# Kernel tuning notes

Measured on AMD Instinct MI355X. Metric: run time of the kernel, lower is better.

The kernel has to match this reference:

```python
import jax, jax.numpy as jnp
import numpy as np

HEAD_DIM = 128  # dim // num_heads; RoPE rot_dim and softmax scale
ROPE_THETA = 10000.0


def rope_rotate(x, rot_dim):
    # lucidrains RotaryEmbedding.rotate_queries_or_keys: rotate first rot_dim
    # channels of last axis with interleaved-pair rotation; pass rest through.
    T = x.shape[-2]
    inv_freq = 1.0 / (ROPE_THETA ** (jnp.arange(0, rot_dim, 2, dtype=jnp.float32) / rot_dim))
    freqs = jnp.arange(T, dtype=jnp.float32)[:, None] * inv_freq[None, :]  # [T, rot_dim//2]
    freqs = jnp.repeat(freqs, 2, axis=-1)  # [T, rot_dim] interleaved (f0,f0,f1,f1,...)
    cos, sin = jnp.cos(freqs), jnp.sin(freqs)
    xr, x_pass = x[..., :rot_dim], x[..., rot_dim:]
    x1, x2 = xr[..., 0::2], xr[..., 1::2]
    rot = jnp.stack([-x2, x1], axis=-1).reshape(xr.shape)  # rotate_half
    xr = xr * cos + rot * sin
    return jnp.concatenate([xr, x_pass], axis=-1)


def setup_inputs() -> dict:
    key = jax.random.key(0)
    ks = jax.random.split(key, 9)
    B, T, D = 2, 2048, 2048
    w = lambda k, shape: jax.random.normal(k, shape, dtype=jnp.float32) * 0.02
    return {
        "latent_space": jax.random.normal(ks[0], (B, T, D), dtype=jnp.float32),
        "Wq": w(ks[1], (D, D)), "bq": w(ks[2], (D,)),
        "Wk": w(ks[3], (D, D)), "bk": w(ks[4], (D,)),
        "Wv": w(ks[5], (D, D)), "bv": w(ks[6], (D,)),
        "Wfc": w(ks[7], (D, D)), "bfc": w(ks[8], (D,)),
    }


def reference(latent_space, Wq, bq, Wk, bk, Wv, bv, Wfc, bfc):
    # Projections (nn.Linear: x @ W.T + b)
    Q = latent_space @ Wq.T + bq
    K = latent_space @ Wk.T + bk
    V = latent_space @ Wv.T + bv
    # Fused RoPE on first HEAD_DIM channels (module never splits heads)
    Q = rope_rotate(Q, HEAD_DIM)
    K = rope_rotate(K, HEAD_DIM)
    # Full-hidden-dim QK^T: [B,T,T]
    qk = jnp.einsum('btd,bsd->bts', Q, K)
    T = qk.shape[-1]
    causal = jnp.triu(jnp.ones((T, T), dtype=bool), 1)
    A = jnp.where(causal, -jnp.inf, qk)
    # PartialSoftmax with temp=1, h_t=None: state = A/sqrt(head_dim);
    # out = exp(state)/sum(exp(state)) * 2
    state = A / jnp.sqrt(jnp.float32(HEAD_DIM))
    x_exp = jnp.exp(state)
    A = x_exp / jnp.sum(x_exp, axis=-1, keepdims=True) * 2.0
    out = jnp.einsum('bts,bsd->btd', A, V) @ Wfc.T + bfc
    return out
```

## Files before the change

kernel.cpp:

```cpp
#include <hip/hip_runtime.h>
#include <hip/hip_bf16.h>
#include <math.h>

using bf16 = __hip_bfloat16;
typedef __attribute__((ext_vector_type(8))) __bf16 bf16x8;
typedef __attribute__((ext_vector_type(4))) float f32x4;

static __device__ __forceinline__ void gload16(const bf16* g, bf16* l) {
  __builtin_amdgcn_global_load_lds((const __attribute__((address_space(1))) void*)g,
                                   (__attribute__((address_space(3))) void*)l, 16, 0, 0);
}

struct POff { long a[4]; long b[4]; long c[4]; const float* bias[4]; };
struct CvtP { const float* s[5]; bf16* d[5]; int n4[5]; };

__global__ __launch_bounds__(256) void cvt_f32_bf16(CvtP p) {
  const int y = blockIdx.y;
  const int i = blockIdx.x * 256 + threadIdx.x;
  if (i >= p.n4[y]) return;
  const float4 v = reinterpret_cast<const float4*>(p.s[y])[i];
  union { bf16 h[4]; short4 s4; } u;
  u.h[0] = __float2bfloat16(v.x);
  u.h[1] = __float2bfloat16(v.y);
  u.h[2] = __float2bfloat16(v.z);
  u.h[3] = __float2bfloat16(v.w);
  *reinterpret_cast<short4*>(p.d[y] + 4 * (size_t)i) = u.s4;
}

template<bool BIAS, bool F32OUT, bool CAUSAL, bool KTRUNC>
__global__ __launch_bounds__(256, 4) void gemm_nt(
    const bf16* __restrict__ A, const bf16* __restrict__ B, char* __restrict__ Cv,
    POff P, int K, int lda, int ldb, int ldc)
{
  if (CAUSAL && blockIdx.x > blockIdx.y) return;
  const int z = blockIdx.z;
  A = (const bf16*)((const char*)A + P.a[z]);
  B = (const bf16*)((const char*)B + P.b[z]);
  char* C = Cv + P.c[z];
  const int by = KTRUNC ? (gridDim.y - 1 - blockIdx.y) : blockIdx.y;
  const int rowBase = by * 128;
  const int colBase = blockIdx.x * 128;
  const int tid  = threadIdx.x;
  const int lane = tid & 63;
  const int wid  = tid >> 6;
  const int wR = (wid >> 1) * 64;
  const int wC = (wid & 1) * 64;

  __shared__ alignas(16) bf16 lsA[128 * 32];
  __shared__ alignas(16) bf16 lsB[128 * 32];

  f32x4 acc[4][4] = {};

  const int kEnd = KTRUNC ? (rowBase + 128) : K;
  const int rt = tid >> 2;
  const int cs = tid & 3;
  const int srcOff = (cs ^ ((rt >> 1) & 3)) * 8;
  const bf16* gA = A + (size_t)(rowBase + rt) * lda + srcOff;
  const bf16* gB = B + (size_t)(colBase + rt) * ldb + srcOff;
  const int lr = lane >> 4;
  const int lc = lane & 15;
  const int kb = (lr ^ ((lc >> 1) & 3)) * 8;

  for (int k0 = 0; k0 < kEnd; k0 += 32) {
    gload16(gA + k0,                    &lsA[tid * 8]);
    gload16(gA + (size_t)64 * lda + k0, &lsA[2048 + tid * 8]);
    gload16(gB + k0,                    &lsB[tid * 8]);
    gload16(gB + (size_t)64 * ldb + k0, &lsB[2048 + tid * 8]);
    __syncthreads();

    bf16x8 af[4], bf_[4];
#pragma unroll
    for (int m = 0; m < 4; ++m)
      af[m] = *reinterpret_cast<const bf16x8*>(&lsA[(wR + m * 16 + lc) * 32 + kb]);
#pragma unroll
    for (int n = 0; n < 4; ++n)
      bf_[n] = *reinterpret_cast<const bf16x8*>(&lsB[(wC + n * 16 + lc) * 32 + kb]);

#pragma unroll
    for (int m = 0; m < 4; ++m)
#pragma unroll
      for (int n = 0; n < 4; ++n)
        acc[m][n] = __builtin_amdgcn_mfma_f32_16x16x32_bf16(af[m], bf_[n], acc[m][n], 0, 0, 0);
    __syncthreads();
  }

  const float* bias = P.bias[z];
#pragma unroll
  for (int m = 0; m < 4; ++m) {
    const int row0 = rowBase + wR + m * 16 + lr * 4;
#pragma unroll
    for (int n = 0; n < 4; ++n) {
      const int col = colBase + wC + n * 16 + lc;
      const float bv = BIAS ? bias[col] : 0.f;
#pragma unroll
      for (int j = 0; j < 4; ++j) {
        const float v = acc[m][n][j] + bv;
        const long idx = (long)(row0 + j) * ldc + col;
        if (F32OUT) reinterpret_cast<float*>(C)[idx] = v;
        else        reinterpret_cast<bf16*>(C)[idx] = __float2bfloat16(v);
      }
    }
  }
}

__global__ __launch_bounds__(256) void rope_bf16(bf16* __restrict__ X) {
  const int idx = blockIdx.x * 256 + threadIdx.x;
  const int row = idx >> 6;
  const int i   = idx & 63;
  const int t   = row & 2047;
  const float ang = (float)t * exp2f((float)i * -0.20762050593046f);
  float sn, cs;
  sincosf(ang, &sn, &cs);
  bf16* p = X + ((long)row << 11) + 2 * i;
  const float x1 = __bfloat162float(p[0]);
  const float x2 = __bfloat162float(p[1]);
  p[0] = __float2bfloat16(x1 * cs - x2 * sn);
  p[1] = __float2bfloat16(x2 * cs + x1 * sn);
}

__global__ __launch_bounds__(256) void softmax_causal(
    const float* __restrict__ S0, const float* __restrict__ S1,
    const float* __restrict__ S2, const float* __restrict__ S3,
    bf16* __restrict__ A0, bf16* __restrict__ A1) {
  const int t = blockIdx.x;
  const int b = blockIdx.y;
  const float* ra = (b ? S2 : S0) + (long)t * 2048;
  const float* rb = (b ? S3 : S1) + (long)t * 2048;
  bf16* orow = (b ? A1 : A0) + (long)t * 4096;
  const int L = t + 1;
  __shared__ float e[2048];
  __shared__ float red[4];
  const float scale = 0.0883883476483184f;
  const int lane = threadIdx.x & 63, wd = threadIdx.x >> 6;

  float mx = -INFINITY;
  for (int s = threadIdx.x; s < L; s += 256) {
    const float v = (ra[s] + rb[s]) * scale;
    e[s] = v;
    mx = fmaxf(mx, v);
  }
#pragma unroll
  for (int off = 1; off < 64; off <<= 1) mx = fmaxf(mx, __shfl_xor(mx, off));
  if (lane == 0) red[wd] = mx;
  __syncthreads();
  mx = fmaxf(fmaxf(red[0], red[1]), fmaxf(red[2], red[3]));
  __syncthreads();

  float sum = 0.f;
  for (int s = threadIdx.x; s < L; s += 256) {
    const float v = expf(e[s] - mx);
    e[s] = v;
    sum += v;
  }
#pragma unroll
  for (int off = 1; off < 64; off <<= 1) sum += __shfl_xor(sum, off);
  if (lane == 0) red[wd] = sum;
  __syncthreads();
  sum = red[0] + red[1] + red[2] + red[3];
  const float f = 2.f / sum;
  for (int s = threadIdx.x; s < 2048; s += 256) {
    const float v = (s < L) ? e[s] * f : 0.f;
    orow[s] = __float2bfloat16(v);
  }
}

__global__ __launch_bounds__(256) void transpose_bf16(
    const bf16* __restrict__ V, bf16* __restrict__ VT) {
  __shared__ bf16 tile[32][33];
  const long b = blockIdx.z;
  const int s0 = blockIdx.y * 32, d0 = blockIdx.x * 32;
  const int tx = threadIdx.x;
  const int ty = threadIdx.y;
  for (int i = ty; i < 32; i += 8)
    tile[i][tx] = V[(b * 2048 + s0 + i) * 2048 + d0 + tx];
  __syncthreads();
  for (int i = ty; i < 32; i += 8)
    VT[(b * 2048 + d0 + i) * 2048 + s0 + tx] = tile[tx][i];
}

extern "C" void kernel_launch(void* const* d_in, const int* in_sizes, int n_in,
                              void* d_out, int out_size, void* d_ws, size_t ws_size,
                              hipStream_t stream) {
  (void)in_sizes; (void)n_in; (void)out_size; (void)ws_size;
  const float* lat = (const float*)d_in[0];
  const float* Wq  = (const float*)d_in[1];
  const float* bq  = (const float*)d_in[2];
  const float* Wk  = (const float*)d_in[3];
  const float* bk  = (const float*)d_in[4];
  const float* Wv  = (const float*)d_in[5];
  const float* bv  = (const float*)d_in[6];
  const float* Wfc = (const float*)d_in[7];
  const float* bfc = (const float*)d_in[8];
  float* out = (float*)d_out;

  constexpr long T = 2048, D = 2048, MT = 4096;
  constexpr long TTB = T * T * 4;
  char* w = (char*)d_ws;
  bf16* latb = (bf16*)w;  w += MT * D * 2;
  bf16* wqb  = (bf16*)w;  w += D * D * 2;
  bf16* wkb  = (bf16*)w;  w += D * D * 2;
  bf16* wvb  = (bf16*)w;  w += D * D * 2;
  bf16* wfb  = (bf16*)w;  w += D * D * 2;
  bf16* Qb   = (bf16*)w;  w += MT * D * 2;
  bf16* Kb   = (bf16*)w;  w += MT * D * 2;
  bf16* Vb   = (bf16*)w;  w += MT * D * 2;
  bf16* VTb  = (bf16*)w;  w += MT * D * 2;
  float* S0  = (float*)w; w += TTB;
  float* S1  = (float*)w; w += TTB;
  float* S2  = (float*)d_out;
  float* S3  = (float*)((char*)d_out + TTB);
  bf16* A0   = (bf16*)S0;
  bf16* A1   = (bf16*)S3;
  bf16* Ob   = latb;

  CvtP cp;
  cp.s[0] = lat; cp.d[0] = latb; cp.n4[0] = (int)(MT * D / 4);
  cp.s[1] = Wq;  cp.d[1] = wqb;  cp.n4[1] = (int)(D * D / 4);
  cp.s[2] = Wk;  cp.d[2] = wkb;  cp.n4[2] = (int)(D * D / 4);
  cp.s[3] = Wv;  cp.d[3] = wvb;  cp.n4[3] = (int)(D * D / 4);
  cp.s[4] = Wfc; cp.d[4] = wfb;  cp.n4[4] = (int)(D * D / 4);
  cvt_f32_bf16<<<dim3(8192, 5), 256, 0, stream>>>(cp);

  POff pq = {};
  for (int z = 0; z < 3; ++z) {
    pq.a[z] = 0;
    pq.b[z] = (long)z * D * D * 2;
    pq.c[z] = (long)z * MT * D * 2;
  }
  pq.bias[0] = bq; pq.bias[1] = bk; pq.bias[2] = bv;
  gemm_nt<true,false,false,false><<<dim3(16, 32, 3), 256, 0, stream>>>(
      latb, wqb, (char*)Qb, pq, 2048, 2048, 2048, 2048);

  rope_bf16<<<2048, 256, 0, stream>>>(Qb);

  POff ps = {};
  for (int z = 0; z < 4; ++z) {
    ps.a[z] = (long)(z >> 1) * T * D * 2 + (long)(z & 1) * 1024 * 2;
    ps.b[z] = ps.a[z];
  }
  ps.c[0] = 0;
  ps.c[1] = TTB;
  ps.c[2] = (char*)S2 - (char*)S0;
  ps.c[3] = (char*)S3 - (char*)S0;
  gemm_nt<false,true,true,false><<<dim3(16, 16, 4), 256, 0, stream>>>(
      Qb, Kb, (char*)S0, ps, 1024, 2048, 2048, 2048);

  softmax_causal<<<dim3(2048, 2), 256, 0, stream>>>(S0, S1, S2, S3, A0, A1);

  transpose_bf16<<<dim3(64, 64, 2), dim3(32, 8), 0, stream>>>(Vb, VTb);

  POff pv = {};
  pv.a[0] = 0; pv.a[1] = (char*)A1 - (char*)A0;
  pv.b[0] = 0; pv.b[1] = (long)D * T * 2;
  pv.c[0] = 0; pv.c[1] = (long)T * D * 2;
  gemm_nt<false,false,false,true><<<dim3(16, 16, 2), 256, 0, stream>>>(
      (const bf16*)A0, VTb, (char*)Ob, pv, 2048, 4096, 2048, 2048);

  POff pf = {};
  pf.bias[0] = bfc;
  gemm_nt<true,true,false,false><<<dim3(16, 32, 1), 256, 0, stream>>>(
      Ob, wfb, (char*)out, pf, 2048, 2048, 2048, 2048);
}
```

Measured before the change: 313.5 us.

## Pipeline GEMM with 4-stage LDS ring buffer and 256x128 tiles of 512 threads

Rewrites the shared GEMM kernel to use 512-thread blocks computing 256x128 tiles, with a 4-deep LDS ring buffer and loads issued three stages ahead. Explicit vmcnt waits and raw barriers replace the double __syncthreads per iteration, and MFMA sections run at raised wave priority. The aim is to hide global-to-LDS latency and halve B-tile loads per output. The trade-off is coarser causal skipping, more LDS per block and fewer blocks per grid.

```diff
diff --git a/kernel.cpp b/kernel.cpp
--- a/kernel.cpp
+++ b/kernel.cpp
@@ -5,6 +5,9 @@
 using bf16 = __hip_bfloat16;
 typedef __attribute__((ext_vector_type(8))) __bf16 bf16x8;
 typedef __attribute__((ext_vector_type(4))) float f32x4;
+
+#define SBAR() asm volatile("s_barrier" ::: "memory")
+#define WAITVM(n) asm volatile("s_waitcnt vmcnt(" #n ")" ::: "memory")
 
 static __device__ __forceinline__ void gload16(const bf16* g, bf16* l) {
   __builtin_amdgcn_global_load_lds((const __attribute__((address_space(1))) void*)g,
@@ -28,69 +31,81 @@
 }
 
 template<bool BIAS, bool F32OUT, bool CAUSAL, bool KTRUNC>
-__global__ __launch_bounds__(256, 4) void gemm_nt(
+__global__ __launch_bounds__(512, 2) void gemm_nt(
     const bf16* __restrict__ A, const bf16* __restrict__ B, char* __restrict__ Cv,
     POff P, int K, int lda, int ldb, int ldc)
 {
-  if (CAUSAL && blockIdx.x > blockIdx.y) return;
+  if (CAUSAL && (int)blockIdx.x > 2 * (int)blockIdx.y + 1) return;
   const int z = blockIdx.z;
   A = (const bf16*)((const char*)A + P.a[z]);
   B = (const bf16*)((const char*)B + P.b[z]);
   char* C = Cv + P.c[z];
-  const int by = KTRUNC ? (gridDim.y - 1 - blockIdx.y) : blockIdx.y;
-  const int rowBase = by * 128;
+  const int by = KTRUNC ? ((int)gridDim.y - 1 - (int)blockIdx.y) : (int)blockIdx.y;
+  const int rowBase = by * 256;
   const int colBase = blockIdx.x * 128;
   const int tid  = threadIdx.x;
   const int lane = tid & 63;
   const int wid  = tid >> 6;
-  const int wR = (wid >> 1) * 64;
-  const int wC = (wid & 1) * 64;
-
-  __shared__ alignas(16) bf16 lsA[128 * 32];
-  __shared__ alignas(16) bf16 lsB[128 * 32];
+  const int wm = wid >> 1;
+  const int wn = wid & 1;
+  const int kEnd = KTRUNC ? (rowBase + 256) : K;
+  const int NT = kEnd >> 5;
+
+  __shared__ alignas(16) bf16 ls[4][12288];
 
   f32x4 acc[4][4] = {};
 
-  const int kEnd = KTRUNC ? (rowBase + 128) : K;
-  const int rt = tid >> 2;
-  const int cs = tid & 3;
-  const int srcOff = (cs ^ ((rt >> 1) & 3)) * 8;
-  const bf16* gA = A + (size_t)(rowBase + rt) * lda + srcOff;
-  const bf16* gB = B + (size_t)(colBase + rt) * ldb + srcOff;
-  const int lr = lane >> 4;
-  const int lc = lane & 15;
+  const int rt  = tid >> 2;
+  const int sw8 = ((tid & 3) ^ ((rt >> 1) & 3)) * 8;
+  const bf16* gA0 = A + (size_t)(rowBase + rt) * lda + sw8;
+  const bf16* gA1 = gA0 + (size_t)128 * lda;
+  const bf16* gB0 = B + (size_t)(colBase + rt) * ldb + sw8;
+
+  const int lr = lane >> 4, lc = lane & 15;
   const int kb = (lr ^ ((lc >> 1) & 3)) * 8;
 
-  for (int k0 = 0; k0 < kEnd; k0 += 32) {
-    gload16(gA + k0,                    &lsA[tid * 8]);
-    gload16(gA + (size_t)64 * lda + k0, &lsA[2048 + tid * 8]);
-    gload16(gB + k0,                    &lsB[tid * 8]);
-    gload16(gB + (size_t)64 * ldb + k0, &lsB[2048 + tid * 8]);
-    __syncthreads();
-
-    bf16x8 af[4], bf_[4];
+#define STAGE(t) { bf16* d = &ls[(t) & 3][0]; const int ko = (t) * 32; \
+    gload16(gA0 + ko, &d[tid * 8]); \
+    gload16(gA1 + ko, &d[4096 + tid * 8]); \
+    gload16(gB0 + ko, &d[8192 + tid * 8]); }
+
+  STAGE(0); STAGE(1); STAGE(2);
+
+  for (int t = 0; t < NT; ++t) {
+    if (t < NT - 2)       WAITVM(6);
+    else if (t == NT - 2) WAITVM(3);
+    else                  WAITVM(0);
+    SBAR();
+    const bf16* LA = &ls[t & 3][0];
+    const bf16* LB = &ls[t & 3][8192];
+    bf16x8 af[4], bfr[4];
 #pragma unroll
     for (int m = 0; m < 4; ++m)
-      af[m] = *reinterpret_cast<const bf16x8*>(&lsA[(wR + m * 16 + lc) * 32 + kb]);
+      af[m] = *reinterpret_cast<const bf16x8*>(&LA[(wm * 64 + m * 16 + lc) * 32 + kb]);
 #pragma unroll
     for (int n = 0; n < 4; ++n)
-      bf_[n] = *reinterpret_cast<const bf16x8*>(&lsB[(wC + n * 16 + lc) * 32 + kb]);
-
+      bfr[n] = *reinterpret_cast<const bf16x8*>(&LB[(wn * 64 + n * 16 + lc) * 32 + kb]);
+    if (t + 3 < NT) STAGE(t + 3);
+    SBAR();
+    __builtin_amdgcn_s_setprio(1);
 #pragma unroll
     for (int m = 0; m < 4; ++m)
 #pragma unroll
       for (int n = 0; n < 4; ++n)
-        acc[m][n] = __builtin_amdgcn_mfma_f32_16x16x32_bf16(af[m], bf_[n], acc[m][n], 0, 0, 0);
-    __syncthreads();
-  }
+        acc[m][n] = __builtin_amdgcn_mfma_f32_16x16x32_bf16(af[m], bfr[n], acc[m][n], 0, 0, 0);
+    __builtin_amdgcn_s_setprio(0);
+  }
+#undef STAGE
 
   const float* bias = P.bias[z];
+  const int crow0 = rowBase + wm * 64;
+  const int ccol0 = colBase + wn * 64;
 #pragma unroll
   for (int m = 0; m < 4; ++m) {
-    const int row0 = rowBase + wR + m * 16 + lr * 4;
+    const int row0 = crow0 + m * 16 + lr * 4;
 #pragma unroll
     for (int n = 0; n < 4; ++n) {
-      const int col = colBase + wC + n * 16 + lc;
+      const int col = ccol0 + n * 16 + lc;
       const float bv = BIAS ? bias[col] : 0.f;
 #pragma unroll
       for (int j = 0; j < 4; ++j) {
@@ -228,7 +243,7 @@
     pq.c[z] = (long)z * MT * D * 2;
   }
   pq.bias[0] = bq; pq.bias[1] = bk; pq.bias[2] = bv;
-  gemm_nt<true,false,false,false><<<dim3(16, 32, 3), 256, 0, stream>>>(
+  gemm_nt<true,false,false,false><<<dim3(16, 16, 3), 512, 0, stream>>>(
       latb, wqb, (char*)Qb, pq, 2048, 2048, 2048, 2048);
 
   rope_bf16<<<2048, 256, 0, stream>>>(Qb);
@@ -242,7 +257,7 @@
   ps.c[1] = TTB;
   ps.c[2] = (char*)S2 - (char*)S0;
   ps.c[3] = (char*)S3 - (char*)S0;
-  gemm_nt<false,true,true,false><<<dim3(16, 16, 4), 256, 0, stream>>>(
+  gemm_nt<false,true,true,false><<<dim3(16, 8, 4), 512, 0, stream>>>(
       Qb, Kb, (char*)S0, ps, 1024, 2048, 2048, 2048);
 
   softmax_causal<<<dim3(2048, 2), 256, 0, stream>>>(S0, S1, S2, S3, A0, A1);
@@ -253,11 +268,11 @@
   pv.a[0] = 0; pv.a[1] = (char*)A1 - (char*)A0;
   pv.b[0] = 0; pv.b[1] = (long)D * T * 2;
   pv.c[0] = 0; pv.c[1] = (long)T * D * 2;
-  gemm_nt<false,false,false,true><<<dim3(16, 16, 2), 256, 0, stream>>>(
+  gemm_nt<false,false,false,true><<<dim3(16, 8, 2), 512, 0, stream>>>(
       (const bf16*)A0, VTb, (char*)Ob, pv, 2048, 4096, 2048, 2048);
 
   POff pf = {};
   pf.bias[0] = bfc;
-  gemm_nt<true,true,false,false><<<dim3(16, 32, 1), 256, 0, stream>>>(
+  gemm_nt<true,true,false,false><<<dim3(16, 16, 1), 512, 0, stream>>>(
       Ob, wfb, (char*)out, pf, 2048, 2048, 2048, 2048);
 }
```

Result: faster. 289.9 us (-7.5%).
